# Kernel tuning notes

Hardware: AMD Instinct MI355X
Metric: run time of the kernel (lower is better)

The kernel has to match this reference:

```python
import jax, jax.numpy as jnp
import numpy as np

N_NODES = 50000


def _gcn_conv(x, edge_index, W, b):
    # x: [N, F_in], edge_index: [2, E] (with self-loops already added)
    n = x.shape[0]
    src, dst = edge_index[0], edge_index[1]
    h = x @ W  # [N, F_out] transform first (as in PyG GCNConv)
    deg = jax.ops.segment_sum(jnp.ones_like(dst, dtype=h.dtype), dst, num_segments=n)
    dinv = jax.lax.rsqrt(jnp.maximum(deg, 1.0))  # self-loops guarantee deg >= 1
    norm = dinv[src] * dinv[dst]  # [E]
    msg = h[src] * norm[:, None]  # [E, F_out] gather + scale
    out = jax.ops.segment_sum(msg, dst, num_segments=n)  # scatter-add to targets
    return out + b


def setup_inputs() -> dict:
    key = jax.random.key(0)
    k1, k2, k3, k4 = jax.random.split(key, 4)
    num_features, hidden, num_classes = 128, 128, 16
    n, e = N_NODES, 800000
    x = jax.random.normal(k1, (n, num_features), dtype=jnp.float32)
    edge_index = jax.random.randint(k2, (2, e), 0, n, dtype=jnp.int64)
    # add self-loops (PyG GCNConv default add_self_loops=True)
    loops = jnp.arange(n, dtype=jnp.int64)
    edge_index = jnp.concatenate([edge_index, jnp.stack([loops, loops])], axis=1)
    s1 = 1.0 / np.sqrt(num_features)
    s2 = 1.0 / np.sqrt(hidden)
    W1 = jax.random.uniform(k3, (num_features, hidden), jnp.float32, -s1, s1)
    b1 = jnp.zeros((hidden,), jnp.float32)
    W2 = jax.random.uniform(k4, (hidden, num_classes), jnp.float32, -s2, s2)
    b2 = jnp.zeros((num_classes,), jnp.float32)
    return {"x": x, "edge_index": edge_index, "W1": W1, "b1": b1, "W2": W2, "b2": b2}


def reference(x, edge_index, W1, b1, W2, b2):
    h = jax.nn.relu(_gcn_conv(x, edge_index, W1, b1))
    # dropout is identity in eval mode (deterministic reference)
    h = _gcn_conv(h, edge_index, W2, b2)
    return jax.nn.log_softmax(h, axis=1)
```

## Files before the change

### kernel.cpp

```cpp
#include <hip/hip_runtime.h>


typedef unsigned int uint32;
typedef unsigned short u16;
typedef __attribute__((ext_vector_type(8))) short bf16x8;
typedef __attribute__((ext_vector_type(4))) float f32x4;

#define NBMAX 1024
#define CHUNK 4096
#define EH 8192

__device__ inline u16 bf16rn(float f) {
    unsigned u = __float_as_uint(f);
    return (u16)((u + 0x7fffu + ((u >> 16) & 1u)) >> 16);
}

__device__ inline void bffma(float2& a, float w, uint32 u) {
    a.x = fmaf(w, __uint_as_float(u << 16), a.x);
    a.y = fmaf(w, __uint_as_float(u & 0xffff0000u), a.y);
}

__global__ __launch_bounds__(256) void k_combo(
    const float* __restrict__ x, const float* __restrict__ W1,
    const int* __restrict__ dstv, int* __restrict__ partials,
    u16* __restrict__ h, int N, int E, int NB, int ntile)
{
    __shared__ __align__(16) unsigned char smem[128 * 136 * 2];
    int t = threadIdx.x;

    if ((int)blockIdx.x >= ntile) {
        int* hl = (int*)smem;
        int hb = blockIdx.x - ntile;
        int e0 = hb * EH, e1 = min(e0 + EH, E);
        for (int i = t; i < NB; i += 256) hl[i] = 0;
        __syncthreads();
        for (int e = e0 + t; e < e1; e += 256)
            atomicAdd(&hl[dstv[e] >> 8], 1);
        __syncthreads();
        int* pr = partials + (size_t)hb * NBMAX;
        for (int i = t; i < NB; i += 256) pr[i] = hl[i];
        return;
    }

    u16* Wl = (u16*)smem;
    const float4* Wg4 = (const float4*)W1;
    for (int g = t; g < 128 * 32; g += 256) {
        int k = g >> 5, n4 = (g & 31) * 4;
        float4 v = Wg4[g];
        Wl[(n4 + 0) * 136 + k] = bf16rn(v.x);
        Wl[(n4 + 1) * 136 + k] = bf16rn(v.y);
        Wl[(n4 + 2) * 136 + k] = bf16rn(v.z);
        Wl[(n4 + 3) * 136 + k] = bf16rn(v.w);
    }
    __syncthreads();

    int wave = t >> 6, lane = t & 63;
    int quad = lane >> 4, ln = lane & 15;
    int rowbase = blockIdx.x * 64 + wave * 16;
    int rclamp = min(rowbase + ln, N - 1);

    f32x4 acc[8];
    #pragma unroll
    for (int ct = 0; ct < 8; ++ct) acc[ct] = (f32x4){0.f, 0.f, 0.f, 0.f};

    #pragma unroll
    for (int q = 0; q < 4; ++q) {
        const float4* xr = (const float4*)(x + (size_t)rclamp * 128 + q * 32 + quad * 8);
        float4 a0 = xr[0], a1 = xr[1];
        bf16x8 afr;
        afr[0] = (short)bf16rn(a0.x); afr[1] = (short)bf16rn(a0.y);
        afr[2] = (short)bf16rn(a0.z); afr[3] = (short)bf16rn(a0.w);
        afr[4] = (short)bf16rn(a1.x); afr[5] = (short)bf16rn(a1.y);
        afr[6] = (short)bf16rn(a1.z); afr[7] = (short)bf16rn(a1.w);
        #pragma unroll
        for (int ct = 0; ct < 8; ++ct) {
            bf16x8 bfr = *(const bf16x8*)&Wl[(ct * 16 + ln) * 136 + q * 32 + quad * 8];
            acc[ct] = __builtin_amdgcn_mfma_f32_16x16x32_bf16(afr, bfr, acc[ct], 0, 0, 0);
        }
    }
    #pragma unroll
    for (int i = 0; i < 4; ++i) {
        int r = rowbase + quad * 4 + i;
        if (r < N) {
            u16* hp = h + (size_t)r * 128 + ln;
            #pragma unroll
            for (int ct = 0; ct < 8; ++ct)
                hp[ct * 16] = bf16rn(acc[ct][i]);
        }
    }
}

__global__ __launch_bounds__(1024) void k_scanB(
    const int* __restrict__ partials, int* __restrict__ bbase,
    int* __restrict__ bfill, int NB, int E, int NH)
{
    __shared__ int s[1024];
    int t = threadIdx.x;
    int v = 0;
    if (t < NB)
        for (int p = 0; p < NH; ++p) v += partials[(size_t)p * NBMAX + t];
    s[t] = v;
    __syncthreads();
    for (int off = 1; off < 1024; off <<= 1) {
        int u = (t >= off) ? s[t - off] : 0;
        __syncthreads();
        s[t] += u;
        __syncthreads();
    }
    if (t < NB) {
        bbase[t] = s[t] - v;
        bfill[t] = 0;
    }
    if (t == 0) bbase[NB] = E;
}

__global__ __launch_bounds__(256) void k_partition(
    const int* __restrict__ src, const int* __restrict__ dstv,
    const int* __restrict__ bbase, int* __restrict__ bfill,
    int2* __restrict__ tmp, int E, int NB)
{
    __shared__ int cntL[NBMAX];
    __shared__ int baseL[NBMAX];
    int t = threadIdx.x;
    int e0 = blockIdx.x * CHUNK;
    int e1 = min(e0 + CHUNK, E);
    for (int i = t; i < NB; i += 256) cntL[i] = 0;
    __syncthreads();
    for (int e = e0 + t; e < e1; e += 256)
        atomicAdd(&cntL[dstv[e] >> 8], 1);
    __syncthreads();
    for (int i = t; i < NB; i += 256) {
        int cc = cntL[i];
        baseL[i] = cc ? bbase[i] + atomicAdd(&bfill[i], cc) : 0;
        cntL[i] = 0;
    }
    __syncthreads();
    for (int e = e0 + t; e < e1; e += 256) {
        int sv = src[e], d = dstv[e];
        int b = d >> 8;
        int r = atomicAdd(&cntL[b], 1);
        tmp[baseL[b] + r] = make_int2(sv, d);
    }
}

__global__ __launch_bounds__(256) void k_bsort(
    const int2* __restrict__ tmp, const int* __restrict__ bbase,
    int* __restrict__ ssrc, int* __restrict__ rs,
    float* __restrict__ dinv, int N)
{
    __shared__ int cnt[256];
    __shared__ int ofs[256];
    int t = threadIdx.x;
    int b = blockIdx.x;
    int base = bbase[b];
    int endb = bbase[b + 1];
    int node0 = b << 8;

    cnt[t] = 0;
    __syncthreads();
    for (int i = base + t; i < endb; i += 256)
        atomicAdd(&cnt[tmp[i].y & 255], 1);
    __syncthreads();
    int v = cnt[t];
    __syncthreads();
    for (int off = 1; off < 256; off <<= 1) {
        int u = (t >= off) ? cnt[t - off] : 0;
        __syncthreads();
        cnt[t] += u;
        __syncthreads();
    }
    int node = node0 + t;
    if (node < N) {
        dinv[node] = rsqrtf(fmaxf((float)v, 1.0f));
        rs[node] = base + cnt[t];
    }
    ofs[t] = base + cnt[t] - v;
    __syncthreads();
    for (int i = base + t; i < endb; i += 256) {
        int2 rec = tmp[i];
        int pos = atomicAdd(&ofs[rec.y & 255], 1);
        ssrc[pos] = rec.x;
    }
}

__global__ __launch_bounds__(256) void k_pull1(
    const int* __restrict__ rs, const int* __restrict__ ssrc,
    const float* __restrict__ dinv, const uint32* __restrict__ h,
    uint32* __restrict__ out1, int N)
{
    int n = (blockIdx.x * 256 + threadIdx.x) >> 6;
    if (n >= N) return;
    int lane = threadIdx.x & 63;
    int start = __builtin_amdgcn_readfirstlane((n == 0) ? 0 : rs[n - 1]);
    int end   = __builtin_amdgcn_readfirstlane(rs[n]);
    float dn = dinv[n];
    float2 a[8];
    #pragma unroll
    for (int i = 0; i < 8; ++i) a[i] = (float2){0.f, 0.f};
    int j = start;
    for (; j + 7 < end; j += 8) {
        int si[8];
        uint32 u[8];
        float w[8];
        #pragma unroll
        for (int i = 0; i < 8; ++i)
            si[i] = __builtin_amdgcn_readfirstlane(ssrc[j + i]);
        #pragma unroll
        for (int i = 0; i < 8; ++i)
            u[i] = h[(size_t)si[i] * 64 + lane];
        #pragma unroll
        for (int i = 0; i < 8; ++i)
            w[i] = dn * dinv[si[i]];
        #pragma unroll
        for (int i = 0; i < 8; ++i)
            bffma(a[i], w[i], u[i]);
    }
    for (; j < end; ++j) {
        int s0 = __builtin_amdgcn_readfirstlane(ssrc[j]);
        bffma(a[0], dn * dinv[s0], h[(size_t)s0 * 64 + lane]);
    }
    float rx = ((a[0].x + a[1].x) + (a[2].x + a[3].x)) +
               ((a[4].x + a[5].x) + (a[6].x + a[7].x));
    float ry = ((a[0].y + a[1].y) + (a[2].y + a[3].y)) +
               ((a[4].y + a[5].y) + (a[6].y + a[7].y));
    out1[(size_t)n * 64 + lane] = ((uint32)bf16rn(ry) << 16) | bf16rn(rx);
}

__global__ __launch_bounds__(256) void k_gemm2(
    const uint32* __restrict__ out1, const float* __restrict__ b1,
    const float* __restrict__ W2, u16* __restrict__ h2, int N)
{
    __shared__ float W2T[16 * 132];
    __shared__ float b1l[128];
    __shared__ float al[32 * 132];
    int t = threadIdx.x;
    int row0 = blockIdx.x * 32;

    for (int g = t; g < 2048; g += 256) {
        int k = g >> 4, f = g & 15;
        W2T[f * 132 + k] = W2[g];
    }
    if (t < 128) b1l[t] = b1[t];
    __syncthreads();

    float4* al4 = (float4*)al;
    const uint4* o4 = (const uint4*)out1;
    for (int g = t; g < 32 * 16; g += 256) {
        int r = g >> 4, k8 = g & 15;
        uint4 u = {0u, 0u, 0u, 0u};
        if (row0 + r < N) u = o4[(size_t)(row0 + r) * 16 + k8];
        const float* bb = &b1l[k8 * 8];
        float4 v0, v1;
        v0.x = fmaxf(__uint_as_float(u.x << 16)         + bb[0], 0.f);
        v0.y = fmaxf(__uint_as_float(u.x & 0xffff0000u) + bb[1], 0.f);
        v0.z = fmaxf(__uint_as_float(u.y << 16)         + bb[2], 0.f);
        v0.w = fmaxf(__uint_as_float(u.y & 0xffff0000u) + bb[3], 0.f);
        v1.x = fmaxf(__uint_as_float(u.z << 16)         + bb[4], 0.f);
        v1.y = fmaxf(__uint_as_float(u.z & 0xffff0000u) + bb[5], 0.f);
        v1.z = fmaxf(__uint_as_float(u.w << 16)         + bb[6], 0.f);
        v1.w = fmaxf(__uint_as_float(u.w & 0xffff0000u) + bb[7], 0.f);
        al4[r * 33 + k8 * 2]     = v0;
        al4[r * 33 + k8 * 2 + 1] = v1;
    }
    __syncthreads();

    int f = t & 15, r0 = t >> 4;
    const float4* W4 = (const float4*)W2T;
    float acc0 = 0.f, acc1 = 0.f;
    #pragma unroll 8
    for (int k4 = 0; k4 < 32; ++k4) {
        float4 w  = W4[f * 33 + k4];
        float4 x0 = al4[r0 * 33 + k4];
        float4 x1 = al4[(r0 + 16) * 33 + k4];
        acc0 = fmaf(x0.x, w.x, acc0); acc0 = fmaf(x0.y, w.y, acc0);
        acc0 = fmaf(x0.z, w.z, acc0); acc0 = fmaf(x0.w, w.w, acc0);
        acc1 = fmaf(x1.x, w.x, acc1); acc1 = fmaf(x1.y, w.y, acc1);
        acc1 = fmaf(x1.z, w.z, acc1); acc1 = fmaf(x1.w, w.w, acc1);
    }
    if (row0 + r0 < N)      h2[(size_t)(row0 + r0) * 16 + f] = bf16rn(acc0);
    if (row0 + r0 + 16 < N) h2[(size_t)(row0 + r0 + 16) * 16 + f] = bf16rn(acc1);
}

__global__ __launch_bounds__(256) void k_pull2(
    const int* __restrict__ rs, const int* __restrict__ ssrc,
    const float* __restrict__ dinv, const uint32* __restrict__ h2,
    const float* __restrict__ b2, float* __restrict__ out, int N)
{
    int idx = blockIdx.x * 256 + threadIdx.x;
    int n = idx >> 3;
    if (n >= N) return;
    int c = idx & 7;
    int start = (n == 0) ? 0 : rs[n - 1];
    int end = rs[n];
    float dn = dinv[n];
    float acc0 = 0.f, acc1 = 0.f;
    for (int j = start; j < end; ++j) {
        int s = ssrc[j];
        float w = dn * dinv[s];
        uint32 u = h2[(size_t)s * 8 + c];
        acc0 = fmaf(w, __uint_as_float(u << 16), acc0);
        acc1 = fmaf(w, __uint_as_float(u & 0xffff0000u), acc1);
    }
    float v0 = acc0 + b2[2 * c];
    float v1 = acc1 + b2[2 * c + 1];
    float m = fmaxf(v0, v1);
    #pragma unroll
    for (int off = 1; off < 8; off <<= 1) m = fmaxf(m, __shfl_xor(m, off));
    float s = expf(v0 - m) + expf(v1 - m);
    #pragma unroll
    for (int off = 1; off < 8; off <<= 1) s += __shfl_xor(s, off);
    float ls = logf(s);
    float2 r = {v0 - m - ls, v1 - m - ls};
    ((float2*)out)[(size_t)n * 8 + c] = r;
}

extern "C" void kernel_launch(void* const* d_in, const int* in_sizes, int n_in,
                              void* d_out, int out_size, void* d_ws, size_t ws_size,
                              hipStream_t stream) {
    const float* x  = (const float*)d_in[0];
    const int*   ei = (const int*)d_in[1];
    const float* W1 = (const float*)d_in[2];
    const float* b1 = (const float*)d_in[3];
    const float* W2 = (const float*)d_in[4];
    const float* b2 = (const float*)d_in[5];
    float* outp = (float*)d_out;

    const int E = in_sizes[1] / 2;
    const int N = in_sizes[0] / 128;
    const int NB = (N + 255) >> 8;
    const int NH = (E + EH - 1) / EH;
    const int ntile = (N + 63) / 64;
    const int* src  = ei;
    const int* dstv = ei + E;

    const int Npad = (N + 255) & ~255;
    const int Epad = (E + 255) & ~255;
    int*   partials = (int*)d_ws;
    int*   bbase = partials + 128 * NBMAX;
    int*   bfill = bbase + NBMAX + 256;
    int*   rs    = bfill + NBMAX;
    float* dinv  = (float*)(rs + Npad);
    int2*  tmp   = (int2*)(dinv + Npad);
    int*   ssrc  = (int*)(tmp + Epad);
    u16*   h     = (u16*)(ssrc + Epad);
    uint32* out1 = (uint32*)(h + (size_t)N * 128);
    u16*   h2    = h;

    k_combo<<<ntile + NH, 256, 0, stream>>>(x, W1, dstv, partials, h, N, E, NB, ntile);
    k_scanB<<<1, 1024, 0, stream>>>(partials, bbase, bfill, NB, E, NH);
    k_partition<<<(E + CHUNK - 1) / CHUNK, 256, 0, stream>>>(src, dstv, bbase,
                                                             bfill, tmp, E, NB);
    k_bsort<<<NB, 256, 0, stream>>>(tmp, bbase, ssrc, rs, dinv, N);
    k_pull1<<<(N * 64 + 255) / 256, 256, 0, stream>>>(rs, ssrc, dinv,
                                                      (const uint32*)h, out1, N);
    k_gemm2<<<(N + 31) / 32, 256, 0, stream>>>(out1, b1, W2, h2, N);
    k_pull2<<<(N * 8 + 255) / 256, 256, 0, stream>>>(rs, ssrc, dinv,
                                                     (const uint32*)h2, b2, outp, N);
}
```

Before: 200.1 us.

## Fuse histogram, scan, partition and bucket sort into persistent combo kernel with grid barriers

The separate scan, partition and bucket-sort kernels are folded into the sort blocks of k_combo. Those blocks now coordinate through global atomic counters and spin-wait barriers, so three kernel launches and their serialization gaps go away. Each chunk builds its local histogram once and reuses it for the partition step instead of recounting. This adds a memset launch and depends on all sort blocks being co-resident; if they are not, the spin-waits can deadlock. The barriers also sit behind GEMM tiles that are scheduled first in the same grid.

```diff
diff --git a/kernel.cpp b/kernel.cpp
--- a/kernel.cpp
+++ b/kernel.cpp
@@ -8,7 +8,6 @@
 
 #define NBMAX 1024
 #define CHUNK 4096
-#define EH 8192
 
 __device__ inline u16 bf16rn(float f) {
     unsigned u = __float_as_uint(f);
@@ -22,23 +21,131 @@
 
 __global__ __launch_bounds__(256) void k_combo(
     const float* __restrict__ x, const float* __restrict__ W1,
-    const int* __restrict__ dstv, int* __restrict__ partials,
-    u16* __restrict__ h, int N, int E, int NB, int ntile)
+    const int* __restrict__ src, const int* __restrict__ dstv,
+    int* __restrict__ bcnt, int* __restrict__ ctl,
+    int* __restrict__ bbase, int* __restrict__ bfill,
+    int2* __restrict__ tmp, int* __restrict__ ssrc,
+    int* __restrict__ rs, float* __restrict__ dinv,
+    u16* __restrict__ h, int N, int E, int NB, int ntile, int NS)
 {
     __shared__ __align__(16) unsigned char smem[128 * 136 * 2];
     int t = threadIdx.x;
 
     if ((int)blockIdx.x >= ntile) {
-        int* hl = (int*)smem;
-        int hb = blockIdx.x - ntile;
-        int e0 = hb * EH, e1 = min(e0 + EH, E);
-        for (int i = t; i < NB; i += 256) hl[i] = 0;
+        int s = blockIdx.x - ntile;
+        int e0 = s * CHUNK, e1 = min(e0 + CHUNK, E);
+        int* cntL = (int*)smem;
+        int* baseL = cntL + NBMAX;
+
+        for (int i = t; i < NB; i += 256) cntL[i] = 0;
         __syncthreads();
         for (int e = e0 + t; e < e1; e += 256)
-            atomicAdd(&hl[dstv[e] >> 8], 1);
-        __syncthreads();
-        int* pr = partials + (size_t)hb * NBMAX;
-        for (int i = t; i < NB; i += 256) pr[i] = hl[i];
+            atomicAdd(&cntL[dstv[e] >> 8], 1);
+        __syncthreads();
+        for (int i = t; i < NB; i += 256)
+            if (cntL[i]) atomicAdd(&bcnt[i], cntL[i]);
+        __syncthreads();
+        if (t == 0)
+            __hip_atomic_fetch_add(&ctl[0], 1, __ATOMIC_ACQ_REL,
+                                   __HIP_MEMORY_SCOPE_AGENT);
+
+        if (s == 0) {
+            if (t == 0)
+                while (__hip_atomic_load(&ctl[0], __ATOMIC_ACQUIRE,
+                                         __HIP_MEMORY_SCOPE_AGENT) < NS)
+                    __builtin_amdgcn_s_sleep(8);
+            __syncthreads();
+            int* sc = baseL;
+            int v[4];
+            int sum = 0;
+            #pragma unroll
+            for (int i = 0; i < 4; ++i) {
+                int idx = t * 4 + i;
+                v[i] = (idx < NB) ? bcnt[idx] : 0;
+                sum += v[i];
+            }
+            sc[t] = sum;
+            __syncthreads();
+            for (int off = 1; off < 256; off <<= 1) {
+                int u = (t >= off) ? sc[t - off] : 0;
+                __syncthreads();
+                sc[t] += u;
+                __syncthreads();
+            }
+            int excl = (t > 0) ? sc[t - 1] : 0;
+            #pragma unroll
+            for (int i = 0; i < 4; ++i) {
+                int idx = t * 4 + i;
+                if (idx < NB) { bbase[idx] = excl; bfill[idx] = 0; }
+                excl += v[i];
+            }
+            if (t == 0) bbase[NB] = E;
+            __threadfence();
+            __syncthreads();
+            if (t == 0)
+                __hip_atomic_store(&ctl[1], 1, __ATOMIC_RELEASE,
+                                   __HIP_MEMORY_SCOPE_AGENT);
+        }
+
+        if (t == 0)
+            while (__hip_atomic_load(&ctl[1], __ATOMIC_ACQUIRE,
+                                     __HIP_MEMORY_SCOPE_AGENT) == 0)
+                __builtin_amdgcn_s_sleep(8);
+        __syncthreads();
+        for (int i = t; i < NB; i += 256) {
+            int c = cntL[i];
+            baseL[i] = c ? bbase[i] + atomicAdd(&bfill[i], c) : 0;
+            cntL[i] = 0;
+        }
+        __syncthreads();
+        for (int e = e0 + t; e < e1; e += 256) {
+            int sv = src[e], d = dstv[e];
+            int b = d >> 8;
+            int r = atomicAdd(&cntL[b], 1);
+            tmp[baseL[b] + r] = make_int2(sv, d);
+        }
+        __threadfence();
+        __syncthreads();
+        if (t == 0)
+            __hip_atomic_fetch_add(&ctl[2], 1, __ATOMIC_ACQ_REL,
+                                   __HIP_MEMORY_SCOPE_AGENT);
+
+        if (s >= NB) return;
+        if (t == 0)
+            while (__hip_atomic_load(&ctl[2], __ATOMIC_ACQUIRE,
+                                     __HIP_MEMORY_SCOPE_AGENT) < NS)
+                __builtin_amdgcn_s_sleep(8);
+        __syncthreads();
+        int* cnt = cntL;
+        int* ofs = cntL + 256;
+        int base = bbase[s];
+        int endb = bbase[s + 1];
+        int node0 = s << 8;
+        cnt[t] = 0;
+        __syncthreads();
+        for (int i = base + t; i < endb; i += 256)
+            atomicAdd(&cnt[tmp[i].y & 255], 1);
+        __syncthreads();
+        int v = cnt[t];
+        __syncthreads();
+        for (int off = 1; off < 256; off <<= 1) {
+            int u = (t >= off) ? cnt[t - off] : 0;
+            __syncthreads();
+            cnt[t] += u;
+            __syncthreads();
+        }
+        int node = node0 + t;
+        if (node < N) {
+            dinv[node] = rsqrtf(fmaxf((float)v, 1.0f));
+            rs[node] = base + cnt[t];
+        }
+        ofs[t] = base + cnt[t] - v;
+        __syncthreads();
+        for (int i = base + t; i < endb; i += 256) {
+            int2 rec = tmp[i];
+            int pos = atomicAdd(&ofs[rec.y & 255], 1);
+            ssrc[pos] = rec.x;
+        }
         return;
     }
 
@@ -87,99 +194,6 @@
             for (int ct = 0; ct < 8; ++ct)
                 hp[ct * 16] = bf16rn(acc[ct][i]);
         }
-    }
-}
-
-__global__ __launch_bounds__(1024) void k_scanB(
-    const int* __restrict__ partials, int* __restrict__ bbase,
-    int* __restrict__ bfill, int NB, int E, int NH)
-{
-    __shared__ int s[1024];
-    int t = threadIdx.x;
-    int v = 0;
-    if (t < NB)
-        for (int p = 0; p < NH; ++p) v += partials[(size_t)p * NBMAX + t];
-    s[t] = v;
-    __syncthreads();
-    for (int off = 1; off < 1024; off <<= 1) {
-        int u = (t >= off) ? s[t - off] : 0;
-        __syncthreads();
-        s[t] += u;
-        __syncthreads();
-    }
-    if (t < NB) {
-        bbase[t] = s[t] - v;
-        bfill[t] = 0;
-    }
-    if (t == 0) bbase[NB] = E;
-}
-
-__global__ __launch_bounds__(256) void k_partition(
-    const int* __restrict__ src, const int* __restrict__ dstv,
-    const int* __restrict__ bbase, int* __restrict__ bfill,
-    int2* __restrict__ tmp, int E, int NB)
-{
-    __shared__ int cntL[NBMAX];
-    __shared__ int baseL[NBMAX];
-    int t = threadIdx.x;
-    int e0 = blockIdx.x * CHUNK;
-    int e1 = min(e0 + CHUNK, E);
-    for (int i = t; i < NB; i += 256) cntL[i] = 0;
-    __syncthreads();
-    for (int e = e0 + t; e < e1; e += 256)
-        atomicAdd(&cntL[dstv[e] >> 8], 1);
-    __syncthreads();
-    for (int i = t; i < NB; i += 256) {
-        int cc = cntL[i];
-        baseL[i] = cc ? bbase[i] + atomicAdd(&bfill[i], cc) : 0;
-        cntL[i] = 0;
-    }
-    __syncthreads();
-    for (int e = e0 + t; e < e1; e += 256) {
-        int sv = src[e], d = dstv[e];
-        int b = d >> 8;
-        int r = atomicAdd(&cntL[b], 1);
-        tmp[baseL[b] + r] = make_int2(sv, d);
-    }
-}
-
-__global__ __launch_bounds__(256) void k_bsort(
-    const int2* __restrict__ tmp, const int* __restrict__ bbase,
-    int* __restrict__ ssrc, int* __restrict__ rs,
-    float* __restrict__ dinv, int N)
-{
-    __shared__ int cnt[256];
-    __shared__ int ofs[256];
-    int t = threadIdx.x;
-    int b = blockIdx.x;
-    int base = bbase[b];
-    int endb = bbase[b + 1];
-    int node0 = b << 8;
-
-    cnt[t] = 0;
-    __syncthreads();
-    for (int i = base + t; i < endb; i += 256)
-        atomicAdd(&cnt[tmp[i].y & 255], 1);
-    __syncthreads();
-    int v = cnt[t];
-    __syncthreads();
-    for (int off = 1; off < 256; off <<= 1) {
-        int u = (t >= off) ? cnt[t - off] : 0;
-        __syncthreads();
-        cnt[t] += u;
-        __syncthreads();
-    }
-    int node = node0 + t;
-    if (node < N) {
-        dinv[node] = rsqrtf(fmaxf((float)v, 1.0f));
-        rs[node] = base + cnt[t];
-    }
-    ofs[t] = base + cnt[t] - v;
-    __syncthreads();
-    for (int i = base + t; i < endb; i += 256) {
-        int2 rec = tmp[i];
-        int pos = atomicAdd(&ofs[rec.y & 255], 1);
-        ssrc[pos] = rec.x;
     }
 }
 
@@ -328,16 +342,18 @@
     const int E = in_sizes[1] / 2;
     const int N = in_sizes[0] / 128;
     const int NB = (N + 255) >> 8;
-    const int NH = (E + EH - 1) / EH;
     const int ntile = (N + 63) / 64;
+    int NS = (E + CHUNK - 1) / CHUNK;
+    if (NS < NB) NS = NB;
     const int* src  = ei;
     const int* dstv = ei + E;
 
     const int Npad = (N + 255) & ~255;
     const int Epad = (E + 255) & ~255;
-    int*   partials = (int*)d_ws;
-    int*   bbase = partials + 128 * NBMAX;
-    int*   bfill = bbase + NBMAX + 256;
+    int*   bcnt  = (int*)d_ws;
+    int*   ctl   = bcnt + NBMAX;
+    int*   bbase = ctl + 8;
+    int*   bfill = bbase + NBMAX + 248;
     int*   rs    = bfill + NBMAX;
     float* dinv  = (float*)(rs + Npad);
     int2*  tmp   = (int2*)(dinv + Npad);
@@ -346,11 +362,11 @@
     uint32* out1 = (uint32*)(h + (size_t)N * 128);
     u16*   h2    = h;
 
-    k_combo<<<ntile + NH, 256, 0, stream>>>(x, W1, dstv, partials, h, N, E, NB, ntile);
-    k_scanB<<<1, 1024, 0, stream>>>(partials, bbase, bfill, NB, E, NH);
-    k_partition<<<(E + CHUNK - 1) / CHUNK, 256, 0, stream>>>(src, dstv, bbase,
-                                                             bfill, tmp, E, NB);
-    k_bsort<<<NB, 256, 0, stream>>>(tmp, bbase, ssrc, rs, dinv, N);
+    hipMemsetAsync(bcnt, 0, (NBMAX + 8) * sizeof(int), stream);
+
+    k_combo<<<ntile + NS, 256, 0, stream>>>(x, W1, src, dstv, bcnt, ctl, bbase,
+                                            bfill, tmp, ssrc, rs, dinv, h,
+                                            N, E, NB, ntile, NS);
     k_pull1<<<(N * 64 + 255) / 256, 256, 0, stream>>>(rs, ssrc, dinv,
                                                       (const uint32*)h, out1, N);
     k_gemm2<<<(N + 31) / 32, 256, 0, stream>>>(out1, b1, W2, h2, N);
```

Result: slower. 265.8 us (+32.9%).

## Sort neighbor lists and band pull1 gathers by source range across rows

Applied to the files above, without the earlier changes.

Each destination's source list is now insertion-sorted in k_bsort. k_pull1 has each wave process 7 rows and walk their neighbor lists in 8 source-index bands, so rows handled together gather h rows from the same region at the same time, aiming for better L2 locality. The cost is a serial per-thread insertion sort, a much smaller grid with fewer waves, loss of the 8-way unrolled independent loads (gathers are now serial per row), and a data-dependent early-exit loop that limits memory-level parallelism.

```diff
diff --git a/kernel.cpp b/kernel.cpp
--- a/kernel.cpp
+++ b/kernel.cpp
@@ -9,6 +9,7 @@
 #define NBMAX 1024
 #define CHUNK 4096
 #define EH 8192
+#define RPW 7
 
 __device__ inline u16 bf16rn(float f) {
     unsigned u = __float_as_uint(f);
@@ -174,56 +175,77 @@
         dinv[node] = rsqrtf(fmaxf((float)v, 1.0f));
         rs[node] = base + cnt[t];
     }
-    ofs[t] = base + cnt[t] - v;
+    int start = base + cnt[t] - v;
+    ofs[t] = start;
     __syncthreads();
     for (int i = base + t; i < endb; i += 256) {
         int2 rec = tmp[i];
         int pos = atomicAdd(&ofs[rec.y & 255], 1);
         ssrc[pos] = rec.x;
     }
+    __syncthreads();
+    for (int i = start + 1; i < start + v; ++i) {
+        int key = ssrc[i];
+        int j = i - 1;
+        while (j >= start && ssrc[j] > key) {
+            ssrc[j + 1] = ssrc[j];
+            --j;
+        }
+        ssrc[j + 1] = key;
+    }
 }
 
 __global__ __launch_bounds__(256) void k_pull1(
     const int* __restrict__ rs, const int* __restrict__ ssrc,
     const float* __restrict__ dinv, const uint32* __restrict__ h,
-    uint32* __restrict__ out1, int N)
-{
-    int n = (blockIdx.x * 256 + threadIdx.x) >> 6;
-    if (n >= N) return;
-    int lane = threadIdx.x & 63;
-    int start = __builtin_amdgcn_readfirstlane((n == 0) ? 0 : rs[n - 1]);
-    int end   = __builtin_amdgcn_readfirstlane(rs[n]);
-    float dn = dinv[n];
-    float2 a[8];
-    #pragma unroll
-    for (int i = 0; i < 8; ++i) a[i] = (float2){0.f, 0.f};
-    int j = start;
-    for (; j + 7 < end; j += 8) {
-        int si[8];
-        uint32 u[8];
-        float w[8];
+    uint32* __restrict__ out1, int N, int BS)
+{
+    int wave = threadIdx.x >> 6, lane = threadIdx.x & 63;
+    int gw = blockIdx.x * 4 + wave;
+    int r0 = gw * RPW;
+    if (r0 >= N) return;
+
+    float2 acc[RPW];
+    int jj[RPW], ee[RPW];
+    float dn[RPW];
+    #pragma unroll
+    for (int i = 0; i < RPW; ++i) {
+        acc[i] = (float2){0.f, 0.f};
+        int n = r0 + i;
+        if (n < N) {
+            jj[i] = __builtin_amdgcn_readfirstlane((n == 0) ? 0 : rs[n - 1]);
+            ee[i] = __builtin_amdgcn_readfirstlane(rs[n]);
+            dn[i] = dinv[n];
+        } else {
+            jj[i] = 0; ee[i] = 0; dn[i] = 0.f;
+        }
+    }
+
+    #pragma unroll
+    for (int b = 0; b < 8; ++b) {
+        int bandEnd = (b == 7) ? 0x7fffffff : (b + 1) * BS;
         #pragma unroll
-        for (int i = 0; i < 8; ++i)
-            si[i] = __builtin_amdgcn_readfirstlane(ssrc[j + i]);
-        #pragma unroll
-        for (int i = 0; i < 8; ++i)
-            u[i] = h[(size_t)si[i] * 64 + lane];
-        #pragma unroll
-        for (int i = 0; i < 8; ++i)
-            w[i] = dn * dinv[si[i]];
-        #pragma unroll
-        for (int i = 0; i < 8; ++i)
-            bffma(a[i], w[i], u[i]);
-    }
-    for (; j < end; ++j) {
-        int s0 = __builtin_amdgcn_readfirstlane(ssrc[j]);
-        bffma(a[0], dn * dinv[s0], h[(size_t)s0 * 64 + lane]);
-    }
-    float rx = ((a[0].x + a[1].x) + (a[2].x + a[3].x)) +
-               ((a[4].x + a[5].x) + (a[6].x + a[7].x));
-    float ry = ((a[0].y + a[1].y) + (a[2].y + a[3].y)) +
-               ((a[4].y + a[5].y) + (a[6].y + a[7].y));
-    out1[(size_t)n * 64 + lane] = ((uint32)bf16rn(ry) << 16) | bf16rn(rx);
+        for (int i = 0; i < RPW; ++i) {
+            int j = jj[i], e = ee[i];
+            float d = dn[i];
+            while (j < e) {
+                int s = __builtin_amdgcn_readfirstlane(ssrc[j]);
+                if (s >= bandEnd) break;
+                float w = d * dinv[s];
+                bffma(acc[i], w, h[(size_t)s * 64 + lane]);
+                ++j;
+            }
+            jj[i] = j;
+        }
+    }
+
+    #pragma unroll
+    for (int i = 0; i < RPW; ++i) {
+        int n = r0 + i;
+        if (n < N)
+            out1[(size_t)n * 64 + lane] =
+                ((uint32)bf16rn(acc[i].y) << 16) | bf16rn(acc[i].x);
+    }
 }
 
 __global__ __launch_bounds__(256) void k_gemm2(
@@ -330,6 +352,7 @@
     const int NB = (N + 255) >> 8;
     const int NH = (E + EH - 1) / EH;
     const int ntile = (N + 63) / 64;
+    const int BS = (N + 7) / 8;
     const int* src  = ei;
     const int* dstv = ei + E;
 
@@ -351,8 +374,8 @@
     k_partition<<<(E + CHUNK - 1) / CHUNK, 256, 0, stream>>>(src, dstv, bbase,
                                                              bfill, tmp, E, NB);
     k_bsort<<<NB, 256, 0, stream>>>(tmp, bbase, ssrc, rs, dinv, N);
-    k_pull1<<<(N * 64 + 255) / 256, 256, 0, stream>>>(rs, ssrc, dinv,
-                                                      (const uint32*)h, out1, N);
+    k_pull1<<<(N + 4 * RPW - 1) / (4 * RPW), 256, 0, stream>>>(
+        rs, ssrc, dinv, (const uint32*)h, out1, N, BS);
     k_gemm2<<<(N + 31) / 32, 256, 0, stream>>>(out1, b1, W2, h2, N);
     k_pull2<<<(N * 8 + 255) / 256, 256, 0, stream>>>(rs, ssrc, dinv,
                                                      (const uint32*)h2, b2, outp, N);
```

Measured after the change: 362.5 us. 81.2% more time.
